# Optimization experiments

Measured on AMD Instinct MI355X. Metric: run time of the kernel, lower is better.

The kernel has to match this reference:

```python
import jax, jax.numpy as jnp
import numpy as np

N = 100000   # nodes
E = 1000000  # edges (avg degree 10)
F_IN, H1, H2, C = 128, 64, 64, 16


def setup_inputs() -> dict:
    key = jax.random.key(0)
    ks = jax.random.split(key, 10)
    x = jax.random.normal(ks[0], (N, F_IN), dtype=jnp.float32)
    edge_src = jax.random.randint(ks[1], (E,), 0, N, dtype=jnp.int32)
    edge_dst = jax.random.randint(ks[2], (E,), 0, N, dtype=jnp.int32)
    # normalized-adjacency-like positive edge weights (~1/deg scale)
    edge_val = jax.random.uniform(ks[3], (E,), dtype=jnp.float32) * 0.1
    def glorot(k, fan_in, fan_out):
        s = np.float32(1.0 / np.sqrt(fan_in))
        return jax.random.normal(k, (fan_in, fan_out), dtype=jnp.float32) * s
    W1 = glorot(ks[4], F_IN, H1)
    W2 = glorot(ks[5], H1, H2)
    W3 = glorot(ks[6], H2, C)
    b1 = jnp.zeros((H1,), jnp.float32)
    b2 = jnp.zeros((H2,), jnp.float32)
    b3 = jnp.zeros((C,), jnp.float32)
    return {"x": x, "edge_val": edge_val, "W1": W1, "b1": b1,
            "W2": W2, "b2": b2, "W3": W3, "b3": b3,
            "edge_src": edge_src, "edge_dst": edge_dst}


def gcn_layer(h, W, b, edge_src, edge_dst, edge_val):
    # support = h @ W ; out = spmm(adj, support) + b
    support = h @ W                                  # [N, d_out]
    msg = support[edge_src] * edge_val[:, None]      # [E, d_out] gather + scale
    agg = jax.ops.segment_sum(msg, edge_dst, num_segments=N)  # scatter-add
    return agg + b


def reference(x, edge_val, W1, b1, W2, b2, W3, b3, edge_src, edge_dst):
    # eval mode: F.dropout(training=False) is identity
    h = jax.nn.relu(gcn_layer(x, W1, b1, edge_src, edge_dst, edge_val))
    h = jax.nn.relu(gcn_layer(h, W2, b2, edge_src, edge_dst, edge_val))
    return gcn_layer(h, W3, b3, edge_src, edge_dst, edge_val)  # [N, C] logits
```

## Files before the change

### kernel.cpp

```cpp
#include <hip/hip_runtime.h>
#include <stdint.h>

#define N_NODES 100000
#define N_EDGES 1000000
#define NBUCK 98
#define CAP 12288

typedef __attribute__((ext_vector_type(8))) __bf16 bf16x8;
typedef __attribute__((ext_vector_type(4))) float f32x4;

static __device__ __forceinline__ float bf2f(unsigned short u) {
    return __uint_as_float(((unsigned int)u) << 16);
}
static __device__ __forceinline__ unsigned short f2bf(float f) {
    unsigned int u = __float_as_uint(f);
    unsigned int r = (u + 0x7FFFu + ((u >> 16) & 1u)) >> 16;
    return (unsigned short)r;
}
static __device__ __forceinline__ float4 ld4_half(const unsigned short* p) {
    ushort4 u = *(const ushort4*)p;
    return make_float4(bf2f(u.x), bf2f(u.y), bf2f(u.z), bf2f(u.w));
}
static __device__ __forceinline__ void st8_half(unsigned short* p, const float* f) {
    int4 u;
    u.x = (int)(((unsigned)f2bf(f[0])) | (((unsigned)f2bf(f[1])) << 16));
    u.y = (int)(((unsigned)f2bf(f[2])) | (((unsigned)f2bf(f[3])) << 16));
    u.z = (int)(((unsigned)f2bf(f[4])) | (((unsigned)f2bf(f[5])) << 16));
    u.w = (int)(((unsigned)f2bf(f[6])) | (((unsigned)f2bf(f[7])) << 16));
    *(int4*)p = u;
}

static __device__ __forceinline__ float ldf(const void* p, size_t i, int bf) {
    return bf ? bf2f(((const unsigned short*)p)[i]) : ((const float*)p)[i];
}

__global__ __launch_bounds__(256) void detect_kernel(const unsigned short* __restrict__ xs,
                                                     int* __restrict__ flag,
                                                     int* __restrict__ bcursor) {
    __shared__ int sz;
    if (threadIdx.x == 0) sz = 0;
    __syncthreads();
    int z = 0;
    for (int i = threadIdx.x; i < 1024; i += 256) {
        float av = fabsf(bf2f(xs[2 * i]));
        if (!(av <= 1048576.0f) || (av != 0.0f && av < 9.5367431640625e-07f)) z++;
    }
    atomicAdd(&sz, z);
    if (threadIdx.x < NBUCK) bcursor[threadIdx.x] = threadIdx.x * CAP;
    __syncthreads();
    if (threadIdx.x == 0) *flag = (sz > 256) ? 0 : 1;
}

__global__ __launch_bounds__(256) void part_kernel(const int* __restrict__ src,
                                                   const int* __restrict__ dst,
                                                   const void* __restrict__ val,
                                                   int* __restrict__ bcursor,
                                                   int2* __restrict__ part,
                                                   const int* __restrict__ flagp) {
    __shared__ int cnt[NBUCK];
    __shared__ int base[NBUCK];
    const int bf = *flagp;
    const int tid = threadIdx.x;
    const int e0 = blockIdx.x * 2048;
    for (int i = tid; i < NBUCK; i += 256) cnt[i] = 0;
    __syncthreads();
    int rank[8], bkt[8], pk[8], vb[8];
#pragma unroll
    for (int i = 0; i < 8; ++i) {
        int e = e0 + i * 256 + tid;
        bkt[i] = -1;
        if (e < N_EDGES) {
            int d = dst[e];
            int b = d >> 10;
            bkt[i] = b;
            pk[i] = src[e] | ((d & 1023) << 17);
            vb[i] = __float_as_int(ldf(val, e, bf));
            rank[i] = atomicAdd(&cnt[b], 1);
        }
    }
    __syncthreads();
    for (int i = tid; i < NBUCK; i += 256) {
        int c = cnt[i];
        base[i] = c ? atomicAdd(&bcursor[i], c) : 0;
    }
    __syncthreads();
#pragma unroll
    for (int i = 0; i < 8; ++i) {
        if (bkt[i] >= 0) part[(size_t)base[bkt[i]] + rank[i]] = make_int2(pk[i], vb[i]);
    }
}

__global__ __launch_bounds__(512) void place_kernel(const int* __restrict__ bcursor,
                                                    const int2* __restrict__ part,
                                                    int* __restrict__ row_start,
                                                    int2* __restrict__ csr_rec) {
    __shared__ int cnt[1024];
    __shared__ int sums[512];
    __shared__ int sh_s, sh_cnt, sh_total;
    const int tid = threadIdx.x;
    const int b = blockIdx.x;
    const int row0 = b << 10;
    const int nrows = min(1024, N_NODES - row0);

    if (tid < 128) sums[tid] = (tid < NBUCK) ? (bcursor[tid] - tid * CAP) : 0;
    __syncthreads();
    for (int off = 1; off < 128; off <<= 1) {
        int t = 0;
        if (tid < 128 && tid >= off) t = sums[tid - off];
        __syncthreads();
        if (tid < 128 && tid >= off) sums[tid] += t;
        __syncthreads();
    }
    if (tid == 0) {
        sh_s = (b > 0) ? sums[b - 1] : 0;
        sh_cnt = bcursor[b] - b * CAP;
        sh_total = sums[NBUCK - 1];
    }
    __syncthreads();
    const int s = sh_s;
    const int cb = sh_cnt;
    const int ps = b * CAP;
    const int total = sh_total;

    for (int i = tid; i < 1024; i += 512) cnt[i] = 0;
    __syncthreads();
    for (int j = tid; j < cb; j += 512) {
        unsigned p = (unsigned)part[ps + j].x;
        atomicAdd(&cnt[p >> 17], 1);
    }
    __syncthreads();
    int a0 = cnt[2 * tid], a1 = cnt[2 * tid + 1];
    int ts = a0 + a1;
    sums[tid] = ts;
    __syncthreads();
    for (int off = 1; off < 512; off <<= 1) {
        int t = 0;
        if (tid >= off) t = sums[tid - off];
        __syncthreads();
        if (tid >= off) sums[tid] += t;
        __syncthreads();
    }
    int excl = sums[tid] - ts;
    cnt[2 * tid] = s + excl;
    cnt[2 * tid + 1] = s + excl + a0;
    if (2 * tid < nrows)     row_start[row0 + 2 * tid] = s + excl;
    if (2 * tid + 1 < nrows) row_start[row0 + 2 * tid + 1] = s + excl + a0;
    if (b == NBUCK - 1 && tid == 0) row_start[N_NODES] = total;
    __syncthreads();
    for (int j = tid; j < cb; j += 512) {
        int2 r = part[ps + j];
        unsigned p = (unsigned)r.x;
        int pos = atomicAdd(&cnt[p >> 17], 1);
        csr_rec[pos] = make_int2((int)(p & 0x1FFFFu), r.y);
    }
}

template <int RS>
static __device__ __forceinline__ void row_gather(const unsigned short* __restrict__ supc,
                                                  const int2* __restrict__ csr_rec,
                                                  int s, int e, float a[8]) {
    if (s >= e) return;
    int2 r[4];
#pragma unroll
    for (int t = 0; t < 4; ++t) r[t] = csr_rec[min(s + t, e - 1)];
    for (int j = s; j < e; j += 4) {
        int4 sp[4];
#pragma unroll
        for (int t = 0; t < 4; ++t) sp[t] = *(const int4*)(supc + (size_t)r[t].x * RS);
        float wv[4];
#pragma unroll
        for (int t = 0; t < 4; ++t) wv[t] = (j + t < e) ? __int_as_float(r[t].y) : 0.0f;
        int jn = j + 4;
        if (jn < e) {
#pragma unroll
            for (int t = 0; t < 4; ++t) r[t] = csr_rec[min(jn + t, e - 1)];
        }
#pragma unroll
        for (int t = 0; t < 4; ++t) {
            float w = wv[t];
            int q[4] = {sp[t].x, sp[t].y, sp[t].z, sp[t].w};
#pragma unroll
            for (int c = 0; c < 4; ++c) {
                float flo = __uint_as_float(((unsigned)q[c]) << 16);
                float fhi = __uint_as_float(((unsigned)q[c]) & 0xffff0000u);
                a[2 * c]     += w * flo;
                a[2 * c + 1] += w * fhi;
            }
        }
    }
}

template <int K, int M, bool DYNIN>
__global__ __launch_bounds__(256) void mgemm_kernel(const void* __restrict__ hv_,
                                                    const void* __restrict__ W,
                                                    unsigned short* __restrict__ out,
                                                    const int* __restrict__ flagp) {
    constexpr int KP = K + 8;
    constexpr int NC = M / 16;
    constexpr int NK = K / 32;

    __shared__ unsigned short wt[M][KP];

    const int bf = *flagp;
    const int tid = threadIdx.x;

    for (int i = tid; i < K * M; i += 256) {
        int k = i / M, m = i % M;
        wt[m][k] = f2bf(ldf(W, i, bf));
    }
    __syncthreads();

    const int lane = tid & 63;
    const int qd = lane >> 4;
    const int ln = lane & 15;
    const int wrow = (tid >> 6) * 16;
    const int tile = blockIdx.x;

    const int row = tile * 64 + wrow + ln;
    const bool ok = row < N_NODES;

    f32x4 acc[NC];
#pragma unroll
    for (int c = 0; c < NC; ++c) acc[c] = (f32x4){0.f, 0.f, 0.f, 0.f};

#pragma unroll
    for (int ks = 0; ks < NK; ++ks) {
        bf16x8 a;
        if (ok) {
            const size_t base = (size_t)row * K + ks * 32 + qd * 8;
            if (DYNIN && !bf) {
                const float* xp = (const float*)hv_ + base;
                float4 f0 = *(const float4*)xp;
                float4 f1 = *(const float4*)(xp + 4);
                ushort4 uu[2];
                uu[0].x = f2bf(f0.x); uu[0].y = f2bf(f0.y); uu[0].z = f2bf(f0.z); uu[0].w = f2bf(f0.w);
                uu[1].x = f2bf(f1.x); uu[1].y = f2bf(f1.y); uu[1].z = f2bf(f1.z); uu[1].w = f2bf(f1.w);
                a = *(const bf16x8*)uu;
            } else {
                a = *(const bf16x8*)((const unsigned short*)hv_ + base);
            }
        } else {
            a = (bf16x8)(__bf16)0.0f;
        }
#pragma unroll
        for (int c = 0; c < NC; ++c) {
            bf16x8 b = *(const bf16x8*)&wt[c * 16 + ln][ks * 32 + qd * 8];
            acc[c] = __builtin_amdgcn_mfma_f32_16x16x32_bf16(a, b, acc[c], 0, 0, 0);
        }
    }

#pragma unroll
    for (int c = 0; c < NC; ++c) {
#pragma unroll
        for (int r = 0; r < 4; ++r) {
            int orow = tile * 64 + wrow + qd * 4 + r;
            if (orow < N_NODES) out[(size_t)orow * M + c * 16 + ln] = f2bf(acc[c][r]);
        }
    }
}

template <int MOUT>
__global__ __launch_bounds__(256, 8) void fused_kernel(const unsigned short* __restrict__ support,
                                                       const int* __restrict__ row_start,
                                                       const int2* __restrict__ csr_rec,
                                                       const void* __restrict__ bias,
                                                       const void* __restrict__ W,
                                                       unsigned short* __restrict__ out,
                                                       const int* __restrict__ flagp) {
    constexpr int K = 64, KP = 72;
    constexpr int NC = MOUT / 16;
    constexpr int NK = 2;

    __shared__ unsigned short agg[64][KP];
    __shared__ unsigned short wt[MOUT][KP];

    const int bf = *flagp;
    const int tid = threadIdx.x;

    for (int i = tid; i < K * MOUT; i += 256) {
        int k = i / MOUT, m = i % MOUT;
        wt[m][k] = f2bf(ldf(W, i, bf));
    }

    const int lane = tid & 63;
    const int qd = lane >> 4;
    const int ln = lane & 15;
    const int wrow = (tid >> 6) * 16;

    const int grp = tid >> 3;
    const int cc = tid & 7;
    float bias8[8];
#pragma unroll
    for (int c = 0; c < 8; ++c) bias8[c] = ldf(bias, cc * 8 + c, bf);
    const unsigned short* supc = support + cc * 8;

    const int tile = blockIdx.x;
#pragma unroll
    for (int p = 0; p < 2; ++p) {
        const int row = tile * 64 + p * 32 + grp;
        int s = row_start[min(row, N_NODES)];
        int e = row_start[min(row + 1, N_NODES)];
        float a[8];
#pragma unroll
        for (int c = 0; c < 8; ++c) a[c] = bias8[c];
        row_gather<64>(supc, csr_rec, s, e, a);
#pragma unroll
        for (int c = 0; c < 8; ++c) a[c] = fmaxf(a[c], 0.f);
        st8_half(&agg[p * 32 + grp][cc * 8], a);
    }
    __syncthreads();

    f32x4 macc[NC];
#pragma unroll
    for (int c = 0; c < NC; ++c) macc[c] = (f32x4){0.f, 0.f, 0.f, 0.f};
#pragma unroll
    for (int ks = 0; ks < NK; ++ks) {
        bf16x8 a = *(const bf16x8*)&agg[wrow + ln][ks * 32 + qd * 8];
#pragma unroll
        for (int c = 0; c < NC; ++c) {
            bf16x8 b = *(const bf16x8*)&wt[c * 16 + ln][ks * 32 + qd * 8];
            macc[c] = __builtin_amdgcn_mfma_f32_16x16x32_bf16(a, b, macc[c], 0, 0, 0);
        }
    }

#pragma unroll
    for (int c = 0; c < NC; ++c) {
#pragma unroll
        for (int r = 0; r < 4; ++r) {
            int orow = tile * 64 + wrow + qd * 4 + r;
            if (orow < N_NODES) out[(size_t)orow * MOUT + c * 16 + ln] = f2bf(macc[c][r]);
        }
    }
}

template <bool DYNOUT>
__global__ __launch_bounds__(256, 8) void spmm16_kernel(const unsigned short* __restrict__ support,
                                                        const int* __restrict__ row_start,
                                                        const int2* __restrict__ csr_rec,
                                                        const void* __restrict__ bias,
                                                        void* __restrict__ out_,
                                                        const int* __restrict__ flagp) {
    constexpr int M = 16;
    int bf = *flagp;
    int tid = threadIdx.x;
    int grp = tid >> 1;
    int cc = tid & 1;
    int row = blockIdx.x * 128 + grp;
    if (row >= N_NODES) return;
    int s = row_start[row];
    int e = row_start[row + 1];
    float a[8];
#pragma unroll
    for (int c = 0; c < 8; ++c) a[c] = ldf(bias, cc * 8 + c, bf);
    row_gather<16>(support + cc * 8, csr_rec, s, e, a);
    if (DYNOUT && !bf) {
        float* op = (float*)out_ + (size_t)row * M + cc * 8;
        *(float4*)op = make_float4(a[0], a[1], a[2], a[3]);
        *(float4*)(op + 4) = make_float4(a[4], a[5], a[6], a[7]);
    } else {
        st8_half((unsigned short*)out_ + (size_t)row * M + cc * 8, a);
    }
}

extern "C" void kernel_launch(void* const* d_in, const int* in_sizes, int n_in,
                              void* d_out, int out_size, void* d_ws, size_t ws_size,
                              hipStream_t stream) {
    (void)in_sizes; (void)n_in; (void)out_size; (void)ws_size;
    const void* x  = d_in[0];
    const void* ev = d_in[1];
    const void* W1 = d_in[2];
    const void* b1 = d_in[3];
    const void* W2 = d_in[4];
    const void* b2 = d_in[5];
    const void* W3 = d_in[6];
    const void* b3 = d_in[7];
    const int* esrc = (const int*)d_in[8];
    const int* edst = (const int*)d_in[9];

    char* ws = (char*)d_ws;
    size_t off = 0;
    auto alloc = [&](size_t bytes) -> void* {
        void* p = ws + off;
        off = (off + bytes + 255) & ~(size_t)255;
        return p;
    };
    unsigned short* A = (unsigned short*)alloc((size_t)N_NODES * 64 * 2);
    unsigned short* B = (unsigned short*)alloc((size_t)N_NODES * 64 * 2);
    int* row_start  = (int*)alloc((size_t)(N_NODES + 1) * 4);
    int* bcursor    = (int*)alloc(512);
    int2* csr_rec   = (int2*)alloc((size_t)N_EDGES * 8);
    int* flagp      = (int*)alloc(256);
    int2* part      = (int2*)A;

    detect_kernel<<<1, 256, 0, stream>>>((const unsigned short*)x, flagp, bcursor);

    part_kernel<<<(N_EDGES + 2047) / 2048, 256, 0, stream>>>(esrc, edst, ev, bcursor, part, flagp);
    place_kernel<<<NBUCK, 512, 0, stream>>>(bcursor, part, row_start, csr_rec);

    const int NT = (N_NODES + 63) / 64;

    mgemm_kernel<128, 64, true><<<NT, 256, 0, stream>>>(x, W1, A, flagp);
    fused_kernel<64><<<NT, 256, 0, stream>>>(A, row_start, csr_rec, b1, W2, B, flagp);
    fused_kernel<16><<<NT, 256, 0, stream>>>(B, row_start, csr_rec, b2, W3, A, flagp);
    spmm16_kernel<true><<<(N_NODES + 127) / 128, 256, 0, stream>>>(A, row_start, csr_rec, b3, d_out, flagp);
}
```

Baseline: 229.2 us.

## Halve CSR bucket size to double place-kernel blocks and hoist row-start loads

Destination buckets for the CSR build shrink from 1024 to 512 rows each, so the placement kernel runs 196 blocks instead of 98 with one row per thread, raising parallelism on a wide GPU. The fused gather kernel now loads the row bounds for both of its rows up front and adds bias after accumulation, which may overlap memory latency. The GEMM kernel also gets a minimum-occupancy launch bound. Per-bucket capacity shrinks to 6656 edges, so an unusually skewed destination distribution could overflow a bucket.

```diff
diff --git a/kernel.cpp b/kernel.cpp
--- a/kernel.cpp
+++ b/kernel.cpp
@@ -3,8 +3,8 @@
 
 #define N_NODES 100000
 #define N_EDGES 1000000
-#define NBUCK 98
-#define CAP 12288
+#define NBUCK 196
+#define CAP 6656
 
 typedef __attribute__((ext_vector_type(8))) __bf16 bf16x8;
 typedef __attribute__((ext_vector_type(4))) float f32x4;
@@ -16,10 +16,6 @@
     unsigned int u = __float_as_uint(f);
     unsigned int r = (u + 0x7FFFu + ((u >> 16) & 1u)) >> 16;
     return (unsigned short)r;
-}
-static __device__ __forceinline__ float4 ld4_half(const unsigned short* p) {
-    ushort4 u = *(const ushort4*)p;
-    return make_float4(bf2f(u.x), bf2f(u.y), bf2f(u.z), bf2f(u.w));
 }
 static __device__ __forceinline__ void st8_half(unsigned short* p, const float* f) {
     int4 u;
@@ -71,9 +67,9 @@
         bkt[i] = -1;
         if (e < N_EDGES) {
             int d = dst[e];
-            int b = d >> 10;
+            int b = d >> 9;
             bkt[i] = b;
-            pk[i] = src[e] | ((d & 1023) << 17);
+            pk[i] = src[e] | ((d & 511) << 17);
             vb[i] = __float_as_int(ldf(val, e, bf));
             rank[i] = atomicAdd(&cnt[b], 1);
         }
@@ -94,21 +90,21 @@
                                                     const int2* __restrict__ part,
                                                     int* __restrict__ row_start,
                                                     int2* __restrict__ csr_rec) {
-    __shared__ int cnt[1024];
+    __shared__ int cnt[512];
     __shared__ int sums[512];
     __shared__ int sh_s, sh_cnt, sh_total;
     const int tid = threadIdx.x;
     const int b = blockIdx.x;
-    const int row0 = b << 10;
-    const int nrows = min(1024, N_NODES - row0);
-
-    if (tid < 128) sums[tid] = (tid < NBUCK) ? (bcursor[tid] - tid * CAP) : 0;
-    __syncthreads();
-    for (int off = 1; off < 128; off <<= 1) {
+    const int row0 = b << 9;
+    const int nrows = min(512, N_NODES - row0);
+
+    if (tid < 256) sums[tid] = (tid < NBUCK) ? (bcursor[tid] - tid * CAP) : 0;
+    __syncthreads();
+    for (int off = 1; off < 256; off <<= 1) {
         int t = 0;
-        if (tid < 128 && tid >= off) t = sums[tid - off];
+        if (tid < 256 && tid >= off) t = sums[tid - off];
         __syncthreads();
-        if (tid < 128 && tid >= off) sums[tid] += t;
+        if (tid < 256 && tid >= off) sums[tid] += t;
         __syncthreads();
     }
     if (tid == 0) {
@@ -122,16 +118,15 @@
     const int ps = b * CAP;
     const int total = sh_total;
 
-    for (int i = tid; i < 1024; i += 512) cnt[i] = 0;
+    cnt[tid] = 0;
     __syncthreads();
     for (int j = tid; j < cb; j += 512) {
         unsigned p = (unsigned)part[ps + j].x;
         atomicAdd(&cnt[p >> 17], 1);
     }
     __syncthreads();
-    int a0 = cnt[2 * tid], a1 = cnt[2 * tid + 1];
-    int ts = a0 + a1;
-    sums[tid] = ts;
+    int own = cnt[tid];
+    sums[tid] = own;
     __syncthreads();
     for (int off = 1; off < 512; off <<= 1) {
         int t = 0;
@@ -140,11 +135,9 @@
         if (tid >= off) sums[tid] += t;
         __syncthreads();
     }
-    int excl = sums[tid] - ts;
-    cnt[2 * tid] = s + excl;
-    cnt[2 * tid + 1] = s + excl + a0;
-    if (2 * tid < nrows)     row_start[row0 + 2 * tid] = s + excl;
-    if (2 * tid + 1 < nrows) row_start[row0 + 2 * tid + 1] = s + excl + a0;
+    int excl = sums[tid] - own;
+    cnt[tid] = s + excl;
+    if (tid < nrows) row_start[row0 + tid] = s + excl;
     if (b == NBUCK - 1 && tid == 0) row_start[N_NODES] = total;
     __syncthreads();
     for (int j = tid; j < cb; j += 512) {
@@ -191,10 +184,10 @@
 }
 
 template <int K, int M, bool DYNIN>
-__global__ __launch_bounds__(256) void mgemm_kernel(const void* __restrict__ hv_,
-                                                    const void* __restrict__ W,
-                                                    unsigned short* __restrict__ out,
-                                                    const int* __restrict__ flagp) {
+__global__ __launch_bounds__(256, 8) void mgemm_kernel(const void* __restrict__ hv_,
+                                                       const void* __restrict__ W,
+                                                       unsigned short* __restrict__ out,
+                                                       const int* __restrict__ flagp) {
     constexpr int KP = K + 8;
     constexpr int NC = M / 16;
     constexpr int NK = K / 32;
@@ -289,24 +282,33 @@
 
     const int grp = tid >> 3;
     const int cc = tid & 7;
-    float bias8[8];
-#pragma unroll
-    for (int c = 0; c < 8; ++c) bias8[c] = ldf(bias, cc * 8 + c, bf);
     const unsigned short* supc = support + cc * 8;
 
     const int tile = blockIdx.x;
-#pragma unroll
-    for (int p = 0; p < 2; ++p) {
-        const int row = tile * 64 + p * 32 + grp;
-        int s = row_start[min(row, N_NODES)];
-        int e = row_start[min(row + 1, N_NODES)];
+    const int rowA = tile * 64 + grp;
+    const int rowB = rowA + 32;
+    int s0 = row_start[min(rowA, N_NODES)];
+    int e0 = row_start[min(rowA + 1, N_NODES)];
+    int s1 = row_start[min(rowB, N_NODES)];
+    int e1 = row_start[min(rowB + 1, N_NODES)];
+
+    {
         float a[8];
 #pragma unroll
-        for (int c = 0; c < 8; ++c) a[c] = bias8[c];
-        row_gather<64>(supc, csr_rec, s, e, a);
-#pragma unroll
-        for (int c = 0; c < 8; ++c) a[c] = fmaxf(a[c], 0.f);
-        st8_half(&agg[p * 32 + grp][cc * 8], a);
+        for (int c = 0; c < 8; ++c) a[c] = 0.0f;
+        row_gather<64>(supc, csr_rec, s0, e0, a);
+#pragma unroll
+        for (int c = 0; c < 8; ++c) a[c] = fmaxf(a[c] + ldf(bias, cc * 8 + c, bf), 0.f);
+        st8_half(&agg[grp][cc * 8], a);
+    }
+    {
+        float a[8];
+#pragma unroll
+        for (int c = 0; c < 8; ++c) a[c] = 0.0f;
+        row_gather<64>(supc, csr_rec, s1, e1, a);
+#pragma unroll
+        for (int c = 0; c < 8; ++c) a[c] = fmaxf(a[c] + ldf(bias, cc * 8 + c, bf), 0.f);
+        st8_half(&agg[32 + grp][cc * 8], a);
     }
     __syncthreads();
 
@@ -351,8 +353,10 @@
     int e = row_start[row + 1];
     float a[8];
 #pragma unroll
-    for (int c = 0; c < 8; ++c) a[c] = ldf(bias, cc * 8 + c, bf);
+    for (int c = 0; c < 8; ++c) a[c] = 0.0f;
     row_gather<16>(support + cc * 8, csr_rec, s, e, a);
+#pragma unroll
+    for (int c = 0; c < 8; ++c) a[c] += ldf(bias, cc * 8 + c, bf);
     if (DYNOUT && !bf) {
         float* op = (float*)out_ + (size_t)row * M + cc * 8;
         *(float4*)op = make_float4(a[0], a[1], a[2], a[3]);
@@ -387,7 +391,7 @@
     unsigned short* A = (unsigned short*)alloc((size_t)N_NODES * 64 * 2);
     unsigned short* B = (unsigned short*)alloc((size_t)N_NODES * 64 * 2);
     int* row_start  = (int*)alloc((size_t)(N_NODES + 1) * 4);
-    int* bcursor    = (int*)alloc(512);
+    int* bcursor    = (int*)alloc(1024);
     int2* csr_rec   = (int2*)alloc((size_t)N_EDGES * 8);
     int* flagp      = (int*)alloc(256);
     int2* part      = (int2*)A;
```

Result: no change. 228.1 us, median of 2 (-0.5%).
